# Performance work log

Measured on AMD Instinct MI355X. Metric: run time of the kernel, lower is better.

## Reference

```python
import jax, jax.numpy as jnp
import numpy as np

B, L, IS, HS, NOPS = 16384, 4, 1024, 512, 3  # batch, mL_w, iS, hS, n_cond_ops


def setup_inputs() -> dict:
    key = jax.random.key(0)
    ks = jax.random.split(key, 8)
    wenc_hs = jax.random.normal(ks[0], (B, L, IS), dtype=jnp.float32)
    wn = jax.random.randint(ks[1], (B,), 0, L + 1, dtype=jnp.int32)
    wc = jax.random.randint(ks[2], (B, L), 0, 8, dtype=jnp.int32)
    # learned params (repeat table is zeros-init in torch; use small randn so it matters)
    repeat = jax.random.normal(ks[3], (L, IS), dtype=jnp.float32) * 0.02
    W1 = jax.random.normal(ks[4], (IS, HS), dtype=jnp.float32) * (1.0 / np.sqrt(IS))
    b1 = jnp.zeros((HS,), dtype=jnp.float32)
    W2 = jax.random.normal(ks[5], (HS, NOPS), dtype=jnp.float32) * (1.0 / np.sqrt(HS))
    b2 = jnp.zeros((NOPS,), dtype=jnp.float32)
    return {"wenc_hs": wenc_hs, "repeat": repeat, "W1": W1, "b1": b1,
            "W2": W2, "b2": b2, "wn": wn, "wc": wc}


def reference(wenc_hs, repeat, W1, b1, W2, b2, wn, wc):
    # rep[b,i] = number of earlier positions j<i with wc[b,j]==wc[b,i]
    eq = wc[:, :, None] == wc[:, None, :]                 # [B, L, L]
    tri = jnp.tril(jnp.ones((L, L), dtype=bool), -1)      # strict lower: j < i
    rep = jnp.sum(eq & tri, axis=-1)                      # [B, L] int, values < L
    add = jnp.where((rep > 0)[:, :, None], repeat[rep], 0.0)  # [B, L, IS]
    valid = (jnp.arange(L)[None, :] < wn[:, None])[:, :, None]  # [B, L, 1]
    x = jnp.where(valid, wenc_hs + add, 0.0)              # ragged pad -> zeros
    # MLP head: Linear -> Dropout(eval: identity) -> Tanh -> Linear
    h = jnp.tanh(jnp.einsum('bli,ih->blh', x, W1) + b1)
    s_wo = jnp.einsum('blh,ho->blo', h, W2) + b2          # [B, L, NOPS]
    return s_wo
```

## Files before the change

### kernel.cpp

```cpp
#include <hip/hip_runtime.h>
#include <hip/hip_bf16.h>
#include <stdint.h>

#define BB    16384
#define LL    4
#define IS    1024
#define HS    512
#define NOPS  3
#define M_TOT (BB*LL)
#define BM    128
#define BK    32
#define NBLK  (M_TOT/BM)
#define KSTEPS (IS/BK)

typedef float  f32x4  __attribute__((ext_vector_type(4)));
typedef short  bf16x8 __attribute__((ext_vector_type(8)));
typedef unsigned short ushort_t;

__device__ __forceinline__ ushort_t f2bf(float f) {
  union { float f; uint32_t u; } v; v.f = f;
  uint32_t r = (v.u + 0x7FFFu + ((v.u >> 16) & 1u)) >> 16;
  return (ushort_t)r;
}

__device__ __forceinline__ float tanh_fast(float x) {
  float e = __expf(2.0f * x);
  return 1.0f - 2.0f * __builtin_amdgcn_rcpf(e + 1.0f);
}

__global__ __launch_bounds__(256) void prep_w1(const float* __restrict__ W1,
                                               ushort_t* __restrict__ wsb) {
  int g    = blockIdx.x * 256 + threadIdx.x;
  int n    = g & (HS - 1);
  int slot = (g >> 9) & 3;
  int kt   = g >> 11;
  int sp   = slot ^ ((n >> 1) & 3);
  bf16x8 u;
#pragma unroll
  for (int j = 0; j < 8; ++j) {
    float f = W1[(size_t)(kt * BK + slot * 8 + j) * HS + n];
    u[j] = (short)f2bf(f);
  }
  *reinterpret_cast<bf16x8*>(&wsb[((size_t)(kt * HS + n) * 4 + sp) * 8]) = u;
}

__global__ __launch_bounds__(512) void fused_main(
    const float* __restrict__ wenc, const float* __restrict__ rep_tab,
    const float* __restrict__ b1,   const float* __restrict__ W2,
    const float* __restrict__ b2,   const int* __restrict__ wn,
    const int* __restrict__ wc,     const ushort_t* __restrict__ wsb,
    float* __restrict__ out) {
  __shared__ __attribute__((aligned(16))) ushort_t As[2][BM * BK];
  __shared__ __attribute__((aligned(16))) ushort_t Bs[2][HS * BK];

  const int t    = threadIdx.x;
  const int lane = t & 63;
  const int wid  = t >> 6;
  const int wm   = wid >> 2;
  const int wnq  = wid & 3;
  const int lr   = lane & 15;
  const int lq   = lane >> 4;
  const int bid  = blockIdx.x;

  const int srow = t >> 2;
  const int sslot = t & 3;
  const int grow = bid * BM + srow;
  const int b_  = grow >> 2;
  const int l_  = grow & 3;
  int c0 = wc[b_ * 4 + 0], c1 = wc[b_ * 4 + 1], c2 = wc[b_ * 4 + 2], c3 = wc[b_ * 4 + 3];
  int me = (l_ == 0) ? c0 : ((l_ == 1) ? c1 : ((l_ == 2) ? c2 : c3));
  int rep = 0;
  if (l_ > 0) rep += (c0 == me);
  if (l_ > 1) rep += (c1 == me);
  if (l_ > 2) rep += (c2 == me);
  const int code = (l_ < wn[b_]) ? rep : -1;
  const float* aptr = wenc + (size_t)grow * IS + sslot * 8;
  const float* rptr = rep_tab + (size_t)rep * IS + sslot * 8;
  const int awoff = srow * BK + ((sslot ^ ((srow >> 1) & 3)) * 8);

  int aoff[4], boff[8];
#pragma unroll
  for (int mi = 0; mi < 4; ++mi) {
    int r = wm * 64 + mi * 16 + lr;
    aoff[mi] = r * BK + ((lq ^ ((r >> 1) & 3)) * 8);
  }
#pragma unroll
  for (int ni = 0; ni < 8; ++ni) {
    int n = wnq * 128 + ni * 16 + lr;
    boff[ni] = n * BK + ((lq ^ ((n >> 1) & 3)) * 8);
  }

  f32x4 acc[4][8];
#pragma unroll
  for (int mi = 0; mi < 4; ++mi)
#pragma unroll
    for (int ni = 0; ni < 8; ++ni) acc[mi][ni] = (f32x4){0.f, 0.f, 0.f, 0.f};

  auto stageB = [&](int buf, int kt) {
    const ushort_t* src = wsb + (size_t)kt * (HS * BK);
#pragma unroll
    for (int i = 0; i < 4; ++i) {
      __builtin_amdgcn_global_load_lds(
          (const __attribute__((address_space(1))) void*)(src + i * 4096 + t * 8),
          (__attribute__((address_space(3))) void*)(&Bs[buf][i * 4096 + t * 8]),
          16, 0, 0);
    }
  };
  auto loadA = [&](int kt, float4& v0, float4& v1) {
    if (code >= 0) {
      const float4* p = reinterpret_cast<const float4*>(aptr + kt * BK);
      v0 = p[0]; v1 = p[1];
      if (code > 0) {
        const float4* q = reinterpret_cast<const float4*>(rptr + kt * BK);
        float4 r0 = q[0], r1 = q[1];
        v0.x += r0.x; v0.y += r0.y; v0.z += r0.z; v0.w += r0.w;
        v1.x += r1.x; v1.y += r1.y; v1.z += r1.z; v1.w += r1.w;
      }
    } else {
      v0 = make_float4(0.f, 0.f, 0.f, 0.f);
      v1 = make_float4(0.f, 0.f, 0.f, 0.f);
    }
  };
  auto writeA = [&](int buf, const float4& v0, const float4& v1) {
    bf16x8 u;
    u[0] = (short)f2bf(v0.x); u[1] = (short)f2bf(v0.y);
    u[2] = (short)f2bf(v0.z); u[3] = (short)f2bf(v0.w);
    u[4] = (short)f2bf(v1.x); u[5] = (short)f2bf(v1.y);
    u[6] = (short)f2bf(v1.z); u[7] = (short)f2bf(v1.w);
    *reinterpret_cast<bf16x8*>(&As[buf][awoff]) = u;
  };
  auto compute = [&](int buf) {
    bf16x8 af[4], bfr[8];
#pragma unroll
    for (int mi = 0; mi < 4; ++mi)
      af[mi] = *reinterpret_cast<const bf16x8*>(&As[buf][aoff[mi]]);
#pragma unroll
    for (int ni = 0; ni < 8; ++ni)
      bfr[ni] = *reinterpret_cast<const bf16x8*>(&Bs[buf][boff[ni]]);
#pragma unroll
    for (int mi = 0; mi < 4; ++mi)
#pragma unroll
      for (int ni = 0; ni < 8; ++ni)
        acc[mi][ni] = __builtin_amdgcn_mfma_f32_16x16x32_bf16(af[mi], bfr[ni],
                                                              acc[mi][ni], 0, 0, 0);
  };

  {
    float4 v0, v1;
    loadA(0, v0, v1);
    stageB(0, 0);
    writeA(0, v0, v1);
  }
  __syncthreads();

#pragma unroll 2
  for (int kt = 0; kt < KSTEPS; ++kt) {
    const int cur = kt & 1, nxt = cur ^ 1;
    const bool more = (kt + 1 < KSTEPS);
    float4 v0, v1;
    if (more) {
      stageB(nxt, kt + 1);
      loadA(kt + 1, v0, v1);
    }
    compute(cur);
    if (more) writeA(nxt, v0, v1);
    __syncthreads();
  }

  float* red = reinterpret_cast<float*>(&As[0][0]);
#pragma unroll
  for (int mi = 0; mi < 4; ++mi) {
    float p[4][3] = {{0.f, 0.f, 0.f}, {0.f, 0.f, 0.f}, {0.f, 0.f, 0.f}, {0.f, 0.f, 0.f}};
#pragma unroll
    for (int ni = 0; ni < 8; ++ni) {
      int n = wnq * 128 + ni * 16 + lr;
      float bv = b1[n];
      float w0 = W2[n * 3 + 0], w1 = W2[n * 3 + 1], w2 = W2[n * 3 + 2];
#pragma unroll
      for (int r = 0; r < 4; ++r) {
        float h = tanh_fast(acc[mi][ni][r] + bv);
        p[r][0] += h * w0; p[r][1] += h * w1; p[r][2] += h * w2;
      }
    }
#pragma unroll
    for (int m = 1; m < 16; m <<= 1) {
#pragma unroll
      for (int r = 0; r < 4; ++r)
#pragma unroll
        for (int o = 0; o < 3; ++o) p[r][o] += __shfl_xor(p[r][o], m, 64);
    }
    if (lr == 0) {
#pragma unroll
      for (int r = 0; r < 4; ++r) {
        int rowl = wm * 64 + mi * 16 + lq * 4 + r;
        red[rowl * 12 + wnq * 3 + 0] = p[r][0];
        red[rowl * 12 + wnq * 3 + 1] = p[r][1];
        red[rowl * 12 + wnq * 3 + 2] = p[r][2];
      }
    }
  }
  __syncthreads();
  if (t < BM * NOPS) {
    int r = t / 3, o = t - r * 3;
    float v = red[r * 12 + 0 + o] + red[r * 12 + 3 + o] +
              red[r * 12 + 6 + o] + red[r * 12 + 9 + o] + b2[o];
    out[(size_t)bid * (BM * NOPS) + t] = v;
  }
}

extern "C" void kernel_launch(void* const* d_in, const int* in_sizes, int n_in,
                              void* d_out, int out_size, void* d_ws, size_t ws_size,
                              hipStream_t stream) {
  const float* wenc    = (const float*)d_in[0];
  const float* rep_tab = (const float*)d_in[1];
  const float* W1      = (const float*)d_in[2];
  const float* b1      = (const float*)d_in[3];
  const float* W2      = (const float*)d_in[4];
  const float* b2      = (const float*)d_in[5];
  const int*   wn      = (const int*)d_in[6];
  const int*   wc      = (const int*)d_in[7];
  float*    outp = (float*)d_out;
  ushort_t* wsb  = (ushort_t*)d_ws;

  prep_w1<<<256, 256, 0, stream>>>(W1, wsb);
  fused_main<<<NBLK, 512, 0, stream>>>(wenc, rep_tab, b1, W2, b2, wn, wc, wsb, outp);
}
```

Baseline: 423.3 us.

## Triple-buffer K loop with manual waitcnt, packed bf16 convert, branchless repeat add

Moves the GEMM main loop from double to triple buffering of the A and B LDS tiles, so loads run two k-steps ahead. Synchronisation now uses hand-placed s_waitcnt vmcnt(8) plus raw s_barrier instead of __syncthreads, with sched_barriers and setprio around the MFMA block. It also replaces the scalar bf16 rounding with the v_cvt_pk_bf16_f32 instruction and makes the repeat-table add branchless through an fma with a 0/1 selector. The cost is more LDS per block (possible occupancy loss), an unconditional load of the repeat row, and brittle manual counter waits.

Measured after the change: 428.4 us. No clear change (+1.2%).

```diff
diff --git a/kernel.cpp b/kernel.cpp
--- a/kernel.cpp
+++ b/kernel.cpp
@@ -12,6 +12,8 @@
 #define BK    32
 #define NBLK  (M_TOT/BM)
 #define KSTEPS (IS/BK)
+#define A_ELEMS (BM*BK)
+#define B_ELEMS (HS*BK)
 
 typedef float  f32x4  __attribute__((ext_vector_type(4)));
 typedef short  bf16x8 __attribute__((ext_vector_type(8)));
@@ -21,6 +23,12 @@
   union { float f; uint32_t u; } v; v.f = f;
   uint32_t r = (v.u + 0x7FFFu + ((v.u >> 16) & 1u)) >> 16;
   return (ushort_t)r;
+}
+
+__device__ __forceinline__ uint32_t cvt_pk(float lo, float hi) {
+  uint32_t r;
+  asm("v_cvt_pk_bf16_f32 %0, %1, %2" : "=v"(r) : "v"(lo), "v"(hi));
+  return r;
 }
 
 __device__ __forceinline__ float tanh_fast(float x) {
@@ -50,8 +58,8 @@
     const float* __restrict__ b2,   const int* __restrict__ wn,
     const int* __restrict__ wc,     const ushort_t* __restrict__ wsb,
     float* __restrict__ out) {
-  __shared__ __attribute__((aligned(16))) ushort_t As[2][BM * BK];
-  __shared__ __attribute__((aligned(16))) ushort_t Bs[2][HS * BK];
+  __shared__ __attribute__((aligned(16))) ushort_t As[3][A_ELEMS];
+  __shared__ __attribute__((aligned(16))) ushort_t Bs[3][B_ELEMS];
 
   const int t    = threadIdx.x;
   const int lane = t & 63;
@@ -62,11 +70,11 @@
   const int lq   = lane >> 4;
   const int bid  = blockIdx.x;
 
-  const int srow = t >> 2;
+  const int srow  = t >> 2;
   const int sslot = t & 3;
-  const int grow = bid * BM + srow;
-  const int b_  = grow >> 2;
-  const int l_  = grow & 3;
+  const int grow  = bid * BM + srow;
+  const int b_ = grow >> 2;
+  const int l_ = grow & 3;
   int c0 = wc[b_ * 4 + 0], c1 = wc[b_ * 4 + 1], c2 = wc[b_ * 4 + 2], c3 = wc[b_ * 4 + 3];
   int me = (l_ == 0) ? c0 : ((l_ == 1) ? c1 : ((l_ == 2) ? c2 : c3));
   int rep = 0;
@@ -74,6 +82,7 @@
   if (l_ > 1) rep += (c1 == me);
   if (l_ > 2) rep += (c2 == me);
   const int code = (l_ < wn[b_]) ? rep : -1;
+  const float sel = (code > 0) ? 1.0f : 0.0f;
   const float* aptr = wenc + (size_t)grow * IS + sslot * 8;
   const float* rptr = rep_tab + (size_t)rep * IS + sslot * 8;
   const int awoff = srow * BK + ((sslot ^ ((srow >> 1) & 3)) * 8);
@@ -97,7 +106,7 @@
     for (int ni = 0; ni < 8; ++ni) acc[mi][ni] = (f32x4){0.f, 0.f, 0.f, 0.f};
 
   auto stageB = [&](int buf, int kt) {
-    const ushort_t* src = wsb + (size_t)kt * (HS * BK);
+    const ushort_t* src = wsb + (size_t)kt * B_ELEMS;
 #pragma unroll
     for (int i = 0; i < 4; ++i) {
       __builtin_amdgcn_global_load_lds(
@@ -106,65 +115,75 @@
           16, 0, 0);
     }
   };
-  auto loadA = [&](int kt, float4& v0, float4& v1) {
+  auto loadA = [&](int kt, float4& v0, float4& v1, float4& r0, float4& r1) {
+    v0 = make_float4(0.f, 0.f, 0.f, 0.f);
+    v1 = make_float4(0.f, 0.f, 0.f, 0.f);
     if (code >= 0) {
       const float4* p = reinterpret_cast<const float4*>(aptr + kt * BK);
       v0 = p[0]; v1 = p[1];
-      if (code > 0) {
-        const float4* q = reinterpret_cast<const float4*>(rptr + kt * BK);
-        float4 r0 = q[0], r1 = q[1];
-        v0.x += r0.x; v0.y += r0.y; v0.z += r0.z; v0.w += r0.w;
-        v1.x += r1.x; v1.y += r1.y; v1.z += r1.z; v1.w += r1.w;
-      }
-    } else {
-      v0 = make_float4(0.f, 0.f, 0.f, 0.f);
-      v1 = make_float4(0.f, 0.f, 0.f, 0.f);
-    }
+    }
+    const float4* q = reinterpret_cast<const float4*>(rptr + kt * BK);
+    r0 = q[0]; r1 = q[1];
   };
-  auto writeA = [&](int buf, const float4& v0, const float4& v1) {
-    bf16x8 u;
-    u[0] = (short)f2bf(v0.x); u[1] = (short)f2bf(v0.y);
-    u[2] = (short)f2bf(v0.z); u[3] = (short)f2bf(v0.w);
-    u[4] = (short)f2bf(v1.x); u[5] = (short)f2bf(v1.y);
-    u[6] = (short)f2bf(v1.z); u[7] = (short)f2bf(v1.w);
-    *reinterpret_cast<bf16x8*>(&As[buf][awoff]) = u;
+  auto writeA = [&](int buf, float4 v0, float4 v1, const float4& r0, const float4& r1) {
+    v0.x = fmaf(r0.x, sel, v0.x); v0.y = fmaf(r0.y, sel, v0.y);
+    v0.z = fmaf(r0.z, sel, v0.z); v0.w = fmaf(r0.w, sel, v0.w);
+    v1.x = fmaf(r1.x, sel, v1.x); v1.y = fmaf(r1.y, sel, v1.y);
+    v1.z = fmaf(r1.z, sel, v1.z); v1.w = fmaf(r1.w, sel, v1.w);
+    uint4 u;
+    u.x = cvt_pk(v0.x, v0.y); u.y = cvt_pk(v0.z, v0.w);
+    u.z = cvt_pk(v1.x, v1.y); u.w = cvt_pk(v1.z, v1.w);
+    *reinterpret_cast<uint4*>(&As[buf][awoff]) = u;
   };
-  auto compute = [&](int buf) {
+
+  {
+    float4 v0, v1, r0, r1;
+    loadA(0, v0, v1, r0, r1);
+    stageB(0, 0);
+    __builtin_amdgcn_sched_barrier(0);
+    writeA(0, v0, v1, r0, r1);
+    loadA(1, v0, v1, r0, r1);
+    stageB(1, 1);
+    __builtin_amdgcn_sched_barrier(0);
+    writeA(1, v0, v1, r0, r1);
+    asm volatile("s_waitcnt vmcnt(8) lgkmcnt(0)" ::: "memory");
+    __builtin_amdgcn_s_barrier();
+  }
+
+#pragma unroll 1
+  for (int kt = 0; kt < KSTEPS; ++kt) {
+    const int cur = kt % 3;
+    const bool pre = (kt + 2 < KSTEPS);
+    float4 v0, v1, r0, r1;
+    if (pre) {
+      loadA(kt + 2, v0, v1, r0, r1);
+      stageB((kt + 2) % 3, kt + 2);
+    }
+    __builtin_amdgcn_sched_barrier(0);
+
     bf16x8 af[4], bfr[8];
 #pragma unroll
     for (int mi = 0; mi < 4; ++mi)
-      af[mi] = *reinterpret_cast<const bf16x8*>(&As[buf][aoff[mi]]);
+      af[mi] = *reinterpret_cast<const bf16x8*>(&As[cur][aoff[mi]]);
 #pragma unroll
     for (int ni = 0; ni < 8; ++ni)
-      bfr[ni] = *reinterpret_cast<const bf16x8*>(&Bs[buf][boff[ni]]);
+      bfr[ni] = *reinterpret_cast<const bf16x8*>(&Bs[cur][boff[ni]]);
+    __builtin_amdgcn_s_setprio(1);
 #pragma unroll
     for (int mi = 0; mi < 4; ++mi)
 #pragma unroll
       for (int ni = 0; ni < 8; ++ni)
         acc[mi][ni] = __builtin_amdgcn_mfma_f32_16x16x32_bf16(af[mi], bfr[ni],
                                                               acc[mi][ni], 0, 0, 0);
-  };
-
-  {
-    float4 v0, v1;
-    loadA(0, v0, v1);
-    stageB(0, 0);
-    writeA(0, v0, v1);
-  }
-  __syncthreads();
-
-#pragma unroll 2
-  for (int kt = 0; kt < KSTEPS; ++kt) {
-    const int cur = kt & 1, nxt = cur ^ 1;
-    const bool more = (kt + 1 < KSTEPS);
-    float4 v0, v1;
-    if (more) {
-      stageB(nxt, kt + 1);
-      loadA(kt + 1, v0, v1);
-    }
-    compute(cur);
-    if (more) writeA(nxt, v0, v1);
-    __syncthreads();
+    __builtin_amdgcn_s_setprio(0);
+
+    if (pre) {
+      writeA((kt + 2) % 3, v0, v1, r0, r1);
+      asm volatile("s_waitcnt vmcnt(8) lgkmcnt(0)" ::: "memory");
+    } else {
+      asm volatile("s_waitcnt vmcnt(0) lgkmcnt(0)" ::: "memory");
+    }
+    __builtin_amdgcn_s_barrier();
   }
 
   float* red = reinterpret_cast<float*>(&As[0][0]);
```
